# Kernel optimization log

Measured on AMD Instinct MI355X. Metric: run time of the kernel, lower is better.

## Reference

```python
import jax, jax.numpy as jnp
import numpy as np

B, N, U, K = 2, 768, 64, 16
D_IN = 2 * U + K  # 144


def setup_inputs() -> dict:
    key = jax.random.key(0)
    ks = jax.random.split(key, 11)
    s = 1.0 / np.sqrt(D_IN)  # torch Linear-style init scale
    return {
        "seq_embed": jax.random.normal(ks[0], (B, N, U), jnp.float32),
        "rel_encoding": jax.random.normal(ks[1], (N, N, K), jnp.float32),
        "rel_mask": jax.random.randint(ks[2], (N, N), 0, 2, jnp.int32),
        "W1_1": jax.random.uniform(ks[3], (D_IN, D_IN), jnp.float32, -s, s),
        "b1_1": jnp.zeros((D_IN,), jnp.float32),
        "W1_2": jax.random.uniform(ks[4], (D_IN, 1), jnp.float32, -s, s),
        "b1_2": jnp.zeros((1,), jnp.float32),
        "W2_1": jax.random.uniform(ks[5], (D_IN, D_IN), jnp.float32, -s, s),
        "b2_1": jnp.zeros((D_IN,), jnp.float32),
        "W2_2": jax.random.uniform(ks[6], (D_IN, 1), jnp.float32, -s, s),
        "b2_2": jnp.zeros((1,), jnp.float32),
    }


def _forward(seq_embed, rel_encoding, rel_mask, params):
    mask = rel_mask.astype(seq_embed.dtype)[None, :, :, None]  # (1,N,N,1)
    deg = rel_mask.astype(seq_embed.dtype).sum(axis=-1)        # (N,)
    b, n, u = seq_embed.shape
    k = rel_encoding.shape[-1]
    for layers in params:  # one iteration per hop
        e_i = jnp.broadcast_to(seq_embed[:, :, None, :], (b, n, n, u))
        e_j = jnp.broadcast_to(seq_embed[:, None, :, :], (b, n, n, u))
        enc = jnp.broadcast_to(rel_encoding[None], (b, n, n, k))
        combined = jnp.concatenate([e_i, e_j, enc], axis=-1)   # (B,N,N,2U+K)
        h = mask * combined
        for (W, bias) in layers:  # small per-edge MLP, LeakyReLU(0.01)
            h = jax.nn.leaky_relu(h @ W + bias)
        w = (mask * h)[..., 0]                                  # (B,N,N)
        scaled = w / deg[None, :, None]                         # divide by D[i]
        # sum_i scaled[b,i,j] * e_j == seq_embed[b,j] * sum_i scaled[b,i,j]
        s = scaled.sum(axis=1)                                  # (B,N)
        seq_embed = s[..., None] * seq_embed                    # (B,N,U)
    return seq_embed


def reference(seq_embed, rel_encoding, rel_mask, W1_1, b1_1, W1_2, b1_2,
              W2_1, b2_1, W2_2, b2_2):
    params = [((W1_1, b1_1), (W1_2, b1_2)), ((W2_1, b2_1), (W2_2, b2_2))]
    return _forward(seq_embed, rel_encoding, rel_mask, params)
```

## Files before the change

### kernel.cpp

```cpp
#include <hip/hip_runtime.h>

typedef __attribute__((ext_vector_type(8))) short bf16x8;
typedef __attribute__((ext_vector_type(16))) float f32x16;
typedef __attribute__((ext_vector_type(4))) float f32x4;

__device__ inline unsigned short f2bf_rne(float x) {
  unsigned u = __float_as_uint(x);
  unsigned r = u + 0x7FFFu + ((u >> 16) & 1u);
  return (unsigned short)(r >> 16);
}
__device__ inline float bf2f(unsigned short h) {
  return __uint_as_float(((unsigned)h) << 16);
}

__global__ __launch_bounds__(256) void pre_kernel(const float* __restrict__ enc,
                                                  unsigned* __restrict__ encpk,
                                                  const int* __restrict__ mask,
                                                  float* __restrict__ mprep) {
  int bid = blockIdx.x;
  if (bid < 9216) {
    int h = bid * 256 + threadIdx.x;
    f32x4 v = *(const f32x4*)(enc + (size_t)h * 4);
    unsigned lo = (unsigned)f2bf_rne(v[0]) | ((unsigned)f2bf_rne(v[1]) << 16);
    unsigned hi = (unsigned)f2bf_rne(v[2]) | ((unsigned)f2bf_rne(v[3]) << 16);
    uint2 o; o.x = lo; o.y = hi;
    *(uint2*)(encpk + (size_t)h * 2) = o;
  } else {
    int i = bid - 9216, t = threadIdx.x;
    int sum = 0;
    for (int j = t; j < 768; j += 256) sum += mask[i*768 + j];
    for (int off = 32; off; off >>= 1) sum += __shfl_down(sum, off, 64);
    __shared__ int part[4];
    __shared__ float inv_s;
    if ((t & 63) == 0) part[t >> 6] = sum;
    __syncthreads();
    if (t == 0) inv_s = 1.0f / (float)(part[0] + part[1] + part[2] + part[3]);
    __syncthreads();
    float inv = inv_s;
    for (int j = t; j < 768; j += 256) mprep[i*768 + j] = (float)mask[i*768 + j] * inv;
  }
}

__global__ __launch_bounds__(256) void prep_kernel(const float* __restrict__ seq,
                                                   const float* __restrict__ W1,
                                                   const float* __restrict__ b1,
                                                   const float* __restrict__ W2,
                                                   unsigned* __restrict__ apk2,
                                                   float* __restrict__ zej,
                                                   unsigned* __restrict__ wpk,
                                                   float* __restrict__ w2pad) {
  const int bi0 = blockIdx.x * 16;
  __shared__ float sq[16][64];
  for (int q = threadIdx.x; q < 16*64; q += 256)
    sq[q >> 6][q & 63] = seq[bi0*64 + q];
  __syncthreads();
  const int c = threadIdx.x;
  if (c < 144) {
    float accA[16], accZ[16];
#pragma unroll
    for (int n = 0; n < 16; ++n) { accA[n] = b1[c]; accZ[n] = 0.f; }
#pragma unroll 4
    for (int u = 0; u < 64; ++u) {
      float wa = W1[u*144 + c];
      float wz = W1[(64 + u)*144 + c];
#pragma unroll
      for (int n = 0; n < 16; ++n) {
        float s = sq[n][u];
        accA[n] = fmaf(s, wa, accA[n]);
        accZ[n] = fmaf(s, wz, accZ[n]);
      }
    }
#pragma unroll
    for (int n = 0; n < 16; ++n) {
      int bi = bi0 + n;
      int b = (bi >= 768) ? 1 : 0;
      int nr = bi - b*768;
      unsigned short hi = f2bf_rne(accA[n]);
      unsigned short lo = f2bf_rne(accA[n] - bf2f(hi));
      apk2[(nr*160 + c)*2 + b] = (unsigned)hi | ((unsigned)lo << 16);
      zej[bi*160 + c] = accZ[n];
    }
  } else if (c < 160) {
#pragma unroll
    for (int n = 0; n < 16; ++n) {
      int bi = bi0 + n;
      int b = (bi >= 768) ? 1 : 0;
      int nr = bi - b*768;
      apk2[(nr*160 + c)*2 + b] = 0u;
      zej[bi*160 + c] = 0.f;
    }
  }
  if (blockIdx.x == 0) {
    for (int g = threadIdx.x; g < 1440; g += 256) {
      if (g < 1280) {
        int ew = g & 3;
        int l = (g >> 2) & 63;
        int t = g >> 8;
        int cc = t*32 + (l & 31);
        unsigned short h[2];
#pragma unroll
        for (int q = 0; q < 2; ++q) {
          int e = ew*2 + q;
          int koff = (l >> 5)*8 + e;
          float v = (cc < 144) ? W1[(128 + koff)*144 + cc] : 0.f;
          h[q] = f2bf_rne(v);
        }
        wpk[g] = (unsigned)h[0] | ((unsigned)h[1] << 16);
      } else {
        int cc = g - 1280;
        w2pad[cc] = (cc < 144) ? W2[cc] : 0.f;
      }
    }
  }
}

__global__ __launch_bounds__(320, 4) void edge_kernel(
    const unsigned* __restrict__ encpk, const uint2* __restrict__ apkp,
    const float* __restrict__ zej, const unsigned* __restrict__ wpk,
    const float* __restrict__ w2pad, const float* __restrict__ b2p,
    const float* __restrict__ mprep, float* __restrict__ s_out) {
  const int tid = threadIdx.x;
  const int lane = tid & 63;
  const int w = tid >> 6;
  const int jb = blockIdx.x;
  const int i0 = blockIdx.y * 24;
  const int l31 = lane & 31, lh = lane >> 5;
  const int jglob = jb*32 + l31;

  bf16x8 wfrag = ((const bf16x8*)wpk)[w*64 + lane];

  float w2own[16];
#pragma unroll
  for (int r = 0; r < 16; ++r)
    w2own[r] = w2pad[w*32 + (r & 3) + 8*(r >> 2) + 4*lh];

  f32x16 Cz0, Cz1;
#pragma unroll
  for (int q = 0; q < 4; ++q) {
    f32x4 z0 = *(const f32x4*)&zej[(0*768 + jglob)*160 + w*32 + 4*lh + 8*q];
    f32x4 z1 = *(const f32x4*)&zej[(768   + jglob)*160 + w*32 + 4*lh + 8*q];
#pragma unroll
    for (int m = 0; m < 4; ++m) { Cz0[q*4 + m] = z0[m]; Cz1[q*4 + m] = z1[m]; }
  }

  float mp[4][2];
  if (tid < 192) {
    const int j = tid & 31, g6 = tid >> 5;
#pragma unroll
    for (int s = 0; s < 4; ++s) {
      int i1 = i0 + s*6 + (g6 >> 1);
      mp[s][0] = mprep[i1*768 + jb*32 + j];
      mp[s][1] = mprep[(i1 + 3)*768 + jb*32 + j];
    }
  } else {
#pragma unroll
    for (int s = 0; s < 4; ++s) { mp[s][0] = 0.f; mp[s][1] = 0.f; }
  }

  bf16x8 ones;
#pragma unroll
  for (int e = 0; e < 8; ++e) ones[e] = 0;
  if (lh == 0) { ones[0] = (short)0x3F80; ones[1] = (short)0x3F80; }

  __shared__ float pdot[5][2][12][32];
  __shared__ float scomb[192];
  __shared__ __align__(16) char lds_enc[5][6][1024];
  const float b2 = *b2p;

  asm volatile("s_waitcnt vmcnt(0)" ::: "memory");
  __builtin_amdgcn_sched_barrier(0);

  uint2 apkv[6];

#define GLD_ENC(I, SLOT)                                                        \
  __builtin_amdgcn_global_load_lds(                                            \
      (const __attribute__((address_space(1))) unsigned*)(encpk +              \
          (size_t)(i0 + (I))*6144 + jb*256 + l31*8 + lh*4),                     \
      (__attribute__((address_space(3))) unsigned*)&lds_enc[w][SLOT][0], 16, 0, 0)
#define APK(I, SLOT) apkv[SLOT] = apkp[(i0 + (I))*160 + w*32 + l31]

  GLD_ENC(0, 0); APK(0, 0);
  GLD_ENC(1, 1); APK(1, 1);
  GLD_ENC(2, 2); APK(2, 2);
  GLD_ENC(3, 3); APK(3, 3);

  float sacc_t = 0.f;

  auto body = [&](int unit, int slot) {
    bf16x8 encf = *(const bf16x8*)(&lds_enc[w][slot][lane*16]);
    uint2 av = apkv[slot];

    f32x16 Ce0 = __builtin_amdgcn_mfma_f32_32x32x16_bf16(wfrag, encf, Cz0, 0, 0, 0);
    f32x16 Ce1 = __builtin_amdgcn_mfma_f32_32x32x16_bf16(wfrag, encf, Cz1, 0, 0, 0);

    bf16x8 af0, af1;
#pragma unroll
    for (int e = 2; e < 8; ++e) { af0[e] = 0; af1[e] = 0; }
    *(unsigned*)&af0 = av.x;
    *(unsigned*)&af1 = av.y;

    f32x16 Cb0 = __builtin_amdgcn_mfma_f32_32x32x16_bf16(af0, ones, Ce0, 0, 0, 0);
    f32x16 Cb1 = __builtin_amdgcn_mfma_f32_32x32x16_bf16(af1, ones, Ce1, 0, 0, 0);

    float ta0[2] = {0.f, 0.f}, tb0[2] = {0.f, 0.f};
    float ta1[2] = {0.f, 0.f}, tb1[2] = {0.f, 0.f};
#pragma unroll
    for (int r = 0; r < 16; ++r) {
      float z0 = Cb0[r], z1 = Cb1[r];
      ta0[r & 1] = fmaf(z0, w2own[r], ta0[r & 1]);
      tb0[r & 1] = fmaf(fabsf(z0), w2own[r], tb0[r & 1]);
      ta1[r & 1] = fmaf(z1, w2own[r], ta1[r & 1]);
      tb1[r & 1] = fmaf(fabsf(z1), w2own[r], tb1[r & 1]);
    }
    float dp0 = 0.505f*(ta0[0] + ta0[1]) + 0.495f*(tb0[0] + tb0[1]);
    float dp1 = 0.505f*(ta1[0] + ta1[1]) + 0.495f*(tb1[0] + tb1[1]);
    pdot[w][lh][unit + 0][l31] = dp0;
    pdot[w][lh][unit + 1][l31] = dp1;
  };

#define STEP(IL, VM)                                                            \
  do {                                                                          \
    if ((IL) < 20) { GLD_ENC((IL) + 4, ((IL) + 4) % 6); APK((IL) + 4, ((IL) + 4) % 6); } \
    asm volatile("s_waitcnt vmcnt(" #VM ")" ::: "memory");                      \
    __builtin_amdgcn_sched_barrier(0);                                          \
    body(((IL) % 6) * 2, (IL) % 6);                                             \
  } while (0)

#define REDUCE(S, LAST)                                                         \
  do {                                                                          \
    asm volatile("s_waitcnt lgkmcnt(0)" ::: "memory");                          \
    __builtin_amdgcn_sched_barrier(0);                                          \
    __builtin_amdgcn_s_barrier();                                               \
    if (tid < 192) {                                                            \
      const int j = tid & 31, g6 = tid >> 5;                                    \
      float s1 = 0.f, s2 = 0.f;                                                 \
      _Pragma("unroll")                                                         \
      for (int w5 = 0; w5 < 5; ++w5) {                                          \
        s1 += pdot[w5][0][g6][j] + pdot[w5][1][g6][j];                          \
        s2 += pdot[w5][0][g6 + 6][j] + pdot[w5][1][g6 + 6][j];                  \
      }                                                                         \
      float wv1 = s1 + b2; wv1 = fmaxf(wv1, 0.01f*wv1);                         \
      float wv2 = s2 + b2; wv2 = fmaxf(wv2, 0.01f*wv2);                         \
      sacc_t = fmaf(mp[S][0], wv1, sacc_t);                                     \
      sacc_t = fmaf(mp[S][1], wv2, sacc_t);                                     \
    }                                                                           \
    if (!(LAST)) {                                                              \
      asm volatile("s_waitcnt lgkmcnt(0)" ::: "memory");                        \
      __builtin_amdgcn_sched_barrier(0);                                        \
      __builtin_amdgcn_s_barrier();                                             \
    }                                                                           \
  } while (0)

  STEP(0, 8);  STEP(1, 8);  STEP(2, 8);  STEP(3, 8);  STEP(4, 8);  STEP(5, 8);
  REDUCE(0, 0);
  STEP(6, 8);  STEP(7, 8);  STEP(8, 8);  STEP(9, 8);  STEP(10, 8); STEP(11, 8);
  REDUCE(1, 0);
  STEP(12, 8); STEP(13, 8); STEP(14, 8); STEP(15, 8); STEP(16, 8); STEP(17, 8);
  REDUCE(2, 0);
  STEP(18, 8); STEP(19, 8); STEP(20, 6); STEP(21, 4); STEP(22, 2); STEP(23, 0);
  REDUCE(3, 1);
#undef STEP
#undef REDUCE
#undef GLD_ENC
#undef APK

  if (tid < 192) scomb[tid] = sacc_t;
  __syncthreads();
  if (tid < 64) {
    const int b = tid >> 5, j = tid & 31;
    float tot = scomb[b*32 + j] + scomb[(b + 2)*32 + j] + scomb[(b + 4)*32 + j];
    atomicAdd(&s_out[b*768 + jb*32 + j], tot);
  }
}

__global__ __launch_bounds__(256) void scale_kernel(const float* __restrict__ s,
                                                    const float* __restrict__ seq_in,
                                                    float* __restrict__ seq_out) {
  int idx = blockIdx.x * 256 + threadIdx.x;
  seq_out[idx] = s[idx >> 6] * seq_in[idx];
}

extern "C" void kernel_launch(void* const* d_in, const int* in_sizes, int n_in,
                              void* d_out, int out_size, void* d_ws, size_t ws_size,
                              hipStream_t stream) {
  const float* seq  = (const float*)d_in[0];
  const float* enc  = (const float*)d_in[1];
  const int*   mask = (const int*)d_in[2];
  const float* W11  = (const float*)d_in[3];
  const float* b11  = (const float*)d_in[4];
  const float* W12  = (const float*)d_in[5];
  const float* b12  = (const float*)d_in[6];
  const float* W21  = (const float*)d_in[7];
  const float* b21  = (const float*)d_in[8];
  const float* W22  = (const float*)d_in[9];
  const float* b22  = (const float*)d_in[10];
  float* out = (float*)d_out;

  float* ws = (float*)d_ws;
  size_t off = 0;
  float* mprep = ws + off;                 off += 768*768;
  unsigned* apk2 = (unsigned*)(ws + off);  off += 2*768*160;
  float* zej = ws + off;                   off += 2*768*160;
  unsigned* wpk = (unsigned*)(ws + off);   off += 1280;
  float* w2pad = ws + off;                 off += 160;
  float* sacc  = ws + off;                 off += 2*768;
  float* seq_mid = ws + off;               off += 2*768*64;
  unsigned* encpk = (unsigned*)(ws + off); off += 768*768*8;

  pre_kernel<<<9984, 256, 0, stream>>>(enc, encpk, mask, mprep);

  prep_kernel<<<96, 256, 0, stream>>>(seq, W11, b11, W12, apk2, zej, wpk, w2pad);
  hipMemsetAsync(sacc, 0, 1536*sizeof(float), stream);
  edge_kernel<<<dim3(24, 32), 320, 0, stream>>>(encpk, (const uint2*)apk2, zej, wpk,
                                                w2pad, b12, mprep, sacc);
  scale_kernel<<<384, 256, 0, stream>>>(sacc, seq, seq_mid);

  prep_kernel<<<96, 256, 0, stream>>>(seq_mid, W21, b21, W22, apk2, zej, wpk, w2pad);
  hipMemsetAsync(sacc, 0, 1536*sizeof(float), stream);
  edge_kernel<<<dim3(24, 32), 320, 0, stream>>>(encpk, (const uint2*)apk2, zej, wpk,
                                                w2pad, b22, mprep, sacc);
  scale_kernel<<<384, 256, 0, stream>>>(sacc, seq_mid, out);
}
```

Before: 116.3 us.

## Fold sacc memset into prep, shrink prefetch ring, pack LeakyReLU epilogue

Several independent changes land together. The hipMemsetAsync of the accumulator is removed and the zeroing is done inside the prep kernel by one block, which saves two launches. The edge kernel's prefetch ring drops from 6 to 4 slots and from 4 to 3 loads in flight, and launch bounds rise from 4 to 5 blocks per SM, trading prefetch depth for occupancy. The second-layer epilogue now applies the LeakyReLU directly with max(z, 0.01z) on packed float2 values, replacing the abs-based decomposition, to cut VALU instructions. The risk is less latency hiding per wave and register pressure under the tighter bound.

```diff
diff --git a/kernel.cpp b/kernel.cpp
--- a/kernel.cpp
+++ b/kernel.cpp
@@ -3,6 +3,7 @@
 typedef __attribute__((ext_vector_type(8))) short bf16x8;
 typedef __attribute__((ext_vector_type(16))) float f32x16;
 typedef __attribute__((ext_vector_type(4))) float f32x4;
+typedef __attribute__((ext_vector_type(2))) float f32x2;
 
 __device__ inline unsigned short f2bf_rne(float x) {
   unsigned u = __float_as_uint(x);
@@ -48,7 +49,8 @@
                                                    unsigned* __restrict__ apk2,
                                                    float* __restrict__ zej,
                                                    unsigned* __restrict__ wpk,
-                                                   float* __restrict__ w2pad) {
+                                                   float* __restrict__ w2pad,
+                                                   float* __restrict__ sacc) {
   const int bi0 = blockIdx.x * 16;
   __shared__ float sq[16][64];
   for (int q = threadIdx.x; q < 16*64; q += 256)
@@ -111,10 +113,12 @@
         w2pad[cc] = (cc < 144) ? W2[cc] : 0.f;
       }
     }
-  }
-}
-
-__global__ __launch_bounds__(320, 4) void edge_kernel(
+  } else if (blockIdx.x == 1) {
+    for (int g = threadIdx.x; g < 1536; g += 256) sacc[g] = 0.f;
+  }
+}
+
+__global__ __launch_bounds__(320, 5) void edge_kernel(
     const unsigned* __restrict__ encpk, const uint2* __restrict__ apkp,
     const float* __restrict__ zej, const unsigned* __restrict__ wpk,
     const float* __restrict__ w2pad, const float* __restrict__ b2p,
@@ -162,15 +166,19 @@
   for (int e = 0; e < 8; ++e) ones[e] = 0;
   if (lh == 0) { ones[0] = (short)0x3F80; ones[1] = (short)0x3F80; }
 
+  uint4 af0u, af1u;
+  af0u.y = af0u.z = af0u.w = 0u;
+  af1u.y = af1u.z = af1u.w = 0u;
+
   __shared__ float pdot[5][2][12][32];
   __shared__ float scomb[192];
-  __shared__ __align__(16) char lds_enc[5][6][1024];
+  __shared__ __align__(16) char lds_enc[5][4][1024];
   const float b2 = *b2p;
 
   asm volatile("s_waitcnt vmcnt(0)" ::: "memory");
   __builtin_amdgcn_sched_barrier(0);
 
-  uint2 apkv[6];
+  uint2 apkv[4];
 
 #define GLD_ENC(I, SLOT)                                                        \
   __builtin_amdgcn_global_load_lds(                                            \
@@ -182,7 +190,6 @@
   GLD_ENC(0, 0); APK(0, 0);
   GLD_ENC(1, 1); APK(1, 1);
   GLD_ENC(2, 2); APK(2, 2);
-  GLD_ENC(3, 3); APK(3, 3);
 
   float sacc_t = 0.f;
 
@@ -193,37 +200,33 @@
     f32x16 Ce0 = __builtin_amdgcn_mfma_f32_32x32x16_bf16(wfrag, encf, Cz0, 0, 0, 0);
     f32x16 Ce1 = __builtin_amdgcn_mfma_f32_32x32x16_bf16(wfrag, encf, Cz1, 0, 0, 0);
 
-    bf16x8 af0, af1;
-#pragma unroll
-    for (int e = 2; e < 8; ++e) { af0[e] = 0; af1[e] = 0; }
-    *(unsigned*)&af0 = av.x;
-    *(unsigned*)&af1 = av.y;
-
-    f32x16 Cb0 = __builtin_amdgcn_mfma_f32_32x32x16_bf16(af0, ones, Ce0, 0, 0, 0);
-    f32x16 Cb1 = __builtin_amdgcn_mfma_f32_32x32x16_bf16(af1, ones, Ce1, 0, 0, 0);
-
-    float ta0[2] = {0.f, 0.f}, tb0[2] = {0.f, 0.f};
-    float ta1[2] = {0.f, 0.f}, tb1[2] = {0.f, 0.f};
+    af0u.x = av.x;
+    af1u.x = av.y;
+    f32x16 Cb0 = __builtin_amdgcn_mfma_f32_32x32x16_bf16(
+        __builtin_bit_cast(bf16x8, af0u), ones, Ce0, 0, 0, 0);
+    f32x16 Cb1 = __builtin_amdgcn_mfma_f32_32x32x16_bf16(
+        __builtin_bit_cast(bf16x8, af1u), ones, Ce1, 0, 0, 0);
+
+    f32x2 acc[4];
+#pragma unroll
+    for (int s = 0; s < 4; ++s) { acc[s][0] = 0.f; acc[s][1] = 0.f; }
 #pragma unroll
     for (int r = 0; r < 16; ++r) {
-      float z0 = Cb0[r], z1 = Cb1[r];
-      ta0[r & 1] = fmaf(z0, w2own[r], ta0[r & 1]);
-      tb0[r & 1] = fmaf(fabsf(z0), w2own[r], tb0[r & 1]);
-      ta1[r & 1] = fmaf(z1, w2own[r], ta1[r & 1]);
-      tb1[r & 1] = fmaf(fabsf(z1), w2own[r], tb1[r & 1]);
-    }
-    float dp0 = 0.505f*(ta0[0] + ta0[1]) + 0.495f*(tb0[0] + tb0[1]);
-    float dp1 = 0.505f*(ta1[0] + ta1[1]) + 0.495f*(tb1[0] + tb1[1]);
-    pdot[w][lh][unit + 0][l31] = dp0;
-    pdot[w][lh][unit + 1][l31] = dp1;
+      f32x2 z2; z2[0] = Cb0[r]; z2[1] = Cb1[r];
+      f32x2 h2 = __builtin_elementwise_max(z2, z2 * 0.01f);
+      acc[r & 3] = h2 * w2own[r] + acc[r & 3];
+    }
+    f32x2 dp = (acc[0] + acc[1]) + (acc[2] + acc[3]);
+    pdot[w][lh][unit + 0][l31] = dp[0];
+    pdot[w][lh][unit + 1][l31] = dp[1];
   };
 
 #define STEP(IL, VM)                                                            \
   do {                                                                          \
-    if ((IL) < 20) { GLD_ENC((IL) + 4, ((IL) + 4) % 6); APK((IL) + 4, ((IL) + 4) % 6); } \
+    if ((IL) < 21) { GLD_ENC((IL) + 3, ((IL) + 3) & 3); APK((IL) + 3, ((IL) + 3) & 3); } \
     asm volatile("s_waitcnt vmcnt(" #VM ")" ::: "memory");                      \
     __builtin_amdgcn_sched_barrier(0);                                          \
-    body(((IL) % 6) * 2, (IL) % 6);                                             \
+    body(((IL) % 6) * 2, (IL) & 3);                                             \
   } while (0)
 
 #define REDUCE(S, LAST)                                                         \
@@ -251,13 +254,13 @@
     }                                                                           \
   } while (0)
 
-  STEP(0, 8);  STEP(1, 8);  STEP(2, 8);  STEP(3, 8);  STEP(4, 8);  STEP(5, 8);
+  STEP(0, 6);  STEP(1, 6);  STEP(2, 6);  STEP(3, 6);  STEP(4, 6);  STEP(5, 6);
   REDUCE(0, 0);
-  STEP(6, 8);  STEP(7, 8);  STEP(8, 8);  STEP(9, 8);  STEP(10, 8); STEP(11, 8);
+  STEP(6, 6);  STEP(7, 6);  STEP(8, 6);  STEP(9, 6);  STEP(10, 6); STEP(11, 6);
   REDUCE(1, 0);
-  STEP(12, 8); STEP(13, 8); STEP(14, 8); STEP(15, 8); STEP(16, 8); STEP(17, 8);
+  STEP(12, 6); STEP(13, 6); STEP(14, 6); STEP(15, 6); STEP(16, 6); STEP(17, 6);
   REDUCE(2, 0);
-  STEP(18, 8); STEP(19, 8); STEP(20, 6); STEP(21, 4); STEP(22, 2); STEP(23, 0);
+  STEP(18, 6); STEP(19, 6); STEP(20, 6); STEP(21, 4); STEP(22, 2); STEP(23, 0);
   REDUCE(3, 1);
 #undef STEP
 #undef REDUCE
@@ -309,14 +312,12 @@
 
   pre_kernel<<<9984, 256, 0, stream>>>(enc, encpk, mask, mprep);
 
-  prep_kernel<<<96, 256, 0, stream>>>(seq, W11, b11, W12, apk2, zej, wpk, w2pad);
-  hipMemsetAsync(sacc, 0, 1536*sizeof(float), stream);
+  prep_kernel<<<96, 256, 0, stream>>>(seq, W11, b11, W12, apk2, zej, wpk, w2pad, sacc);
   edge_kernel<<<dim3(24, 32), 320, 0, stream>>>(encpk, (const uint2*)apk2, zej, wpk,
                                                 w2pad, b12, mprep, sacc);
   scale_kernel<<<384, 256, 0, stream>>>(sacc, seq, seq_mid);
 
-  prep_kernel<<<96, 256, 0, stream>>>(seq_mid, W21, b21, W22, apk2, zej, wpk, w2pad);
-  hipMemsetAsync(sacc, 0, 1536*sizeof(float), stream);
+  prep_kernel<<<96, 256, 0, stream>>>(seq_mid, W21, b21, W22, apk2, zej, wpk, w2pad, sacc);
   edge_kernel<<<dim3(24, 32), 320, 0, stream>>>(encpk, (const uint2*)apk2, zej, wpk,
                                                 w2pad, b22, mprep, sacc);
   scale_kernel<<<384, 256, 0, stream>>>(sacc, seq_mid, out);
```

New measurement: 431.3 us. +270.7%, slower.
